# Performance work log

Measured on AMD Instinct MI355X. Metric: run time of the kernel, lower is better.

## Reference

```python
import jax, jax.numpy as jnp
import numpy as np

B, S, D = 2, 2048, 512
H = 8
HD = D // H  # head dim = 64


def setup_inputs() -> dict:
    key = jax.random.key(0)
    ks = jax.random.split(key, 4)
    scale = 1.0 / np.sqrt(D)
    x = jax.random.normal(ks[0], (B, S, D), dtype=jnp.float32)
    wq = jax.random.normal(ks[1], (D, D), dtype=jnp.float32) * scale
    wk = jax.random.normal(ks[2], (D, D), dtype=jnp.float32) * scale
    wv = jax.random.normal(ks[3], (D, D), dtype=jnp.float32) * scale
    bq = jnp.zeros((D,), dtype=jnp.float32)
    bk = jnp.zeros((D,), dtype=jnp.float32)
    bv = jnp.zeros((D,), dtype=jnp.float32)
    return {"x": x, "wq": wq, "bq": bq, "wk": wk, "bk": bk, "wv": wv, "bv": bv}


def reference(x, wq, bq, wk, bk, wv, bv):
    # Linear projections (torch Linear: y = x @ W^T + b; weights here stored as [out,in])
    q = x @ wq.T + bq  # [B,S,D]
    k = x @ wk.T + bk
    v = x @ wv.T + bv
    # split heads -> [B,H,S,HD]
    q = q.reshape(B, S, H, HD).transpose(0, 2, 1, 3)
    k = k.reshape(B, S, H, HD).transpose(0, 2, 1, 3)
    v = v.reshape(B, S, H, HD).transpose(0, 2, 1, 3)
    # QK^T scores, scaled by 1/sqrt(head_dim)
    scores = jnp.einsum("bhqd,bhkd->bhqk", q, k) / jnp.sqrt(jnp.float32(HD))
    # softmax-free: elementwise sigmoid instead of softmax normalization
    attn = jax.nn.sigmoid(scores)  # [B,H,S,S] — the memory-bound intermediate
    out = jnp.einsum("bhqk,bhkd->bhqd", attn, v)
    # merge heads -> [B,S,D]
    return out.transpose(0, 2, 1, 3).reshape(B, S, D)
```

## Files before the change

### kernel.cpp

```cpp
#include <hip/hip_runtime.h>
#include <cstdint>
#include <cstddef>

#define BB   2
#define SS   2048
#define DD   512
#define HH   8
#define HDIM 64
#define XN   ((size_t)BB * SS * DD)
#define WN   ((size_t)DD * DD)

typedef __attribute__((ext_vector_type(8)))  short          s16x8;
typedef __attribute__((ext_vector_type(8)))  unsigned short u16x8;
typedef __attribute__((ext_vector_type(16))) float          f32x16;

static __device__ __forceinline__ unsigned short f2bf(float f) {
  union { float f; unsigned u; } x; x.f = f;
  unsigned r = x.u + 0x7fffu + ((x.u >> 16) & 1u);
  return (unsigned short)(r >> 16);
}
static __device__ __forceinline__ unsigned packtrunc(float lo, float hi) {
  return __builtin_amdgcn_perm(__float_as_uint(hi), __float_as_uint(lo), 0x07060302u);
}

#define QSCALE (-0.18033688011111543f)

__global__ __launch_bounds__(256) void cvt_kernel(
    const float* __restrict__ x,
    const float* __restrict__ wq, const float* __restrict__ wk, const float* __restrict__ wv,
    unsigned short* __restrict__ xb, unsigned short* __restrict__ wb3) {
  const int y = blockIdx.y;
  const float* src; unsigned short* dst;
  if (y == 0) { src = x; dst = xb; }
  else {
    if (blockIdx.x >= 256) return;
    src = (y == 1) ? wq : (y == 2) ? wk : wv;
    dst = wb3 + (size_t)(y - 1) * WN;
  }
  int i = (blockIdx.x * 256 + threadIdx.x) * 4;
  float4 f = *(const float4*)(src + i);
  ushort4 o;
  o.x = f2bf(f.x); o.y = f2bf(f.y); o.z = f2bf(f.z); o.w = f2bf(f.w);
  *(ushort4*)(dst + i) = o;
}

__global__ __launch_bounds__(256) void proj_kernel(
    const unsigned short* __restrict__ xb, const unsigned short* __restrict__ wb3,
    const float* __restrict__ bq, const float* __restrict__ bk, const float* __restrict__ bv,
    unsigned short* __restrict__ qo, unsigned short* __restrict__ ko,
    unsigned short* __restrict__ vt) {
  __shared__ unsigned short As[2][128 * 40];
  __shared__ unsigned short Bs[2][64 * 40];

  const int z = blockIdx.z;
  const unsigned short* w = wb3 + (size_t)z * WN;
  const float* bias = (z == 0) ? bq : (z == 1) ? bk : bv;

  const int t = threadIdx.x;
  const int lane = t & 63, wave = t >> 6;
  const int ln = lane & 31, hi = lane >> 5;
  const int m0 = blockIdx.x * 128, n0 = blockIdx.y * 64;

  u16x8 ar[2], br;
#pragma unroll
  for (int i = 0; i < 2; i++) {
    int c = t + i * 256;
    ar[i] = *(const u16x8*)&xb[(size_t)(m0 + (c >> 2)) * DD + (c & 3) * 8];
  }
  br = *(const u16x8*)&w[(size_t)(n0 + (t >> 2)) * DD + (t & 3) * 8];
#pragma unroll
  for (int i = 0; i < 2; i++) {
    int c = t + i * 256;
    *(u16x8*)&As[0][(c >> 2) * 40 + (c & 3) * 8] = ar[i];
  }
  *(u16x8*)&Bs[0][(t >> 2) * 40 + (t & 3) * 8] = br;
  __syncthreads();

  f32x16 acc0 = {}, acc1 = {};

#pragma unroll 2
  for (int kt = 0; kt < 16; kt++) {
    const int cur = kt & 1, nxt = cur ^ 1;
    if (kt < 15) {
      int k0 = (kt + 1) * 32;
#pragma unroll
      for (int i = 0; i < 2; i++) {
        int c = t + i * 256;
        ar[i] = *(const u16x8*)&xb[(size_t)(m0 + (c >> 2)) * DD + k0 + (c & 3) * 8];
      }
      br = *(const u16x8*)&w[(size_t)(n0 + (t >> 2)) * DD + k0 + (t & 3) * 8];
    }
#pragma unroll
    for (int cc = 0; cc < 2; cc++) {
      s16x8 af = *(const s16x8*)&As[cur][(wave * 32 + ln) * 40 + cc * 16 + hi * 8];
      s16x8 b0 = *(const s16x8*)&Bs[cur][(ln) * 40 + cc * 16 + hi * 8];
      s16x8 b1 = *(const s16x8*)&Bs[cur][(32 + ln) * 40 + cc * 16 + hi * 8];
      acc0 = __builtin_amdgcn_mfma_f32_32x32x16_bf16(af, b0, acc0, 0, 0, 0);
      acc1 = __builtin_amdgcn_mfma_f32_32x32x16_bf16(af, b1, acc1, 0, 0, 0);
    }
    if (kt < 15) {
#pragma unroll
      for (int i = 0; i < 2; i++) {
        int c = t + i * 256;
        *(u16x8*)&As[nxt][(c >> 2) * 40 + (c & 3) * 8] = ar[i];
      }
      *(u16x8*)&Bs[nxt][(t >> 2) * 40 + (t & 3) * 8] = br;
    }
    __syncthreads();
  }

  const int h = blockIdx.y;
  const int bidx = m0 >> 11;
  const int sbase = (m0 & 2047) + wave * 32;
  const size_t bhb = (size_t)(bidx * HH + h) * SS * HDIM;
  const int kts = sbase >> 5;

#pragma unroll
  for (int nh = 0; nh < 2; nh++) {
    f32x16 acc = nh ? acc1 : acc0;
    const int hd = nh * 32 + ln;
    const float bval = bias[n0 + hd];

    if (z == 0) {
#pragma unroll
      for (int r = 0; r < 16; r++) {
        int s = sbase + (r & 3) + 8 * (r >> 2) + 4 * hi;
        qo[bhb + (size_t)s * HDIM + hd] = f2bf((acc[r] + bval) * QSCALE);
      }
    } else if (z == 1) {
      const int c = hd >> 4, hk = (hd >> 3) & 1, j = hd & 7;
      unsigned short* kd = ko + bhb + ((size_t)kts * 4 + c) * 512 + j;
#pragma unroll
      for (int r = 0; r < 16; r++) {
        int off = (r & 3) + 8 * (r >> 2) + 4 * hi;
        kd[(hk * 32 + off) * 8] = f2bf(acc[r] + bval);
      }
    } else {
      unsigned short* vd = vt + bhb + ((size_t)kts * 4 + nh * 2) * 512 + hi * 256 + ln * 8;
#pragma unroll
      for (int g = 0; g < 4; g++) {
        unsigned short* vg = vd + (g >> 1) * 512 + (g & 1) * 4;
#pragma unroll
        for (int j = 0; j < 4; j += 2) {
          unsigned pk = (unsigned)f2bf(acc[g * 4 + j] + bval) |
                        ((unsigned)f2bf(acc[g * 4 + j + 1] + bval) << 16);
          *(unsigned*)&vg[j] = pk;
        }
      }
    }
  }
}

__global__ __launch_bounds__(512, 2) void attn_kernel(
    const unsigned short* __restrict__ qb,
    const unsigned short* __restrict__ kfb,
    const unsigned short* __restrict__ vfb,
    float* __restrict__ out) {
  __shared__ __align__(16) float red[2 * 8192];

  const int t = threadIdx.x;
  const int lane = t & 63, wave = t >> 6;
  const int ln = lane & 31, hi = lane >> 5;
  const int qp = wave & 1, kh = wave >> 1;
  const int fid = blockIdx.y * 16 + blockIdx.x;
  const int bh = fid & 15, qx = fid >> 4;
  const int b = bh >> 3, h = bh & 7;
  const unsigned short* qp_ = qb + (size_t)bh * SS * HDIM;
  const unsigned short* kfp = kfb + (size_t)bh * SS * HDIM;
  const unsigned short* vfp = vfb + (size_t)bh * SS * HDIM;
  const int q0 = qx * 128 + qp * 64;

  s16x8 qf[2][4];
#pragma unroll
  for (int qs = 0; qs < 2; qs++)
#pragma unroll
    for (int c = 0; c < 4; c++)
      qf[qs][c] = *(const s16x8*)&qp_[(size_t)(q0 + qs * 32 + ln) * HDIM + c * 16 + hi * 8];

  f32x16 o00 = {}, o01 = {}, o10 = {}, o11 = {};

  s16x8 kf[4], vf[4];
  int foff = kh * 16 * 2048 + lane * 8;
#pragma unroll
  for (int c = 0; c < 4; c++) {
    kf[c] = *(const s16x8*)&kfp[foff + c * 512];
    vf[c] = *(const s16x8*)&vfp[foff + c * 512];
  }
  foff += 2048;

#pragma unroll 1
  for (int i = 0; i < 16; i++) {
    f32x16 st0 = {}, st1 = {};
#pragma unroll
    for (int c = 0; c < 4; c++) {
      st0 = __builtin_amdgcn_mfma_f32_32x32x16_bf16(kf[c], qf[0][c], st0, 0, 0, 0);
      st1 = __builtin_amdgcn_mfma_f32_32x32x16_bf16(kf[c], qf[1][c], st1, 0, 0, 0);
    }

    if (i < 15) {
#pragma unroll
      for (int c = 0; c < 4; c++)
        kf[c] = *(const s16x8*)&kfp[foff + c * 512];
    }

    unsigned pg[2][8];
#pragma unroll
    for (int qs = 0; qs < 2; qs++) {
      f32x16 st = qs ? st1 : st0;
#pragma unroll
      for (int g = 0; g < 4; g++) {
        float p0 = __builtin_amdgcn_rcpf(1.0f + __builtin_amdgcn_exp2f(st[4 * g + 0]));
        float p1 = __builtin_amdgcn_rcpf(1.0f + __builtin_amdgcn_exp2f(st[4 * g + 1]));
        float p2 = __builtin_amdgcn_rcpf(1.0f + __builtin_amdgcn_exp2f(st[4 * g + 2]));
        float p3 = __builtin_amdgcn_rcpf(1.0f + __builtin_amdgcn_exp2f(st[4 * g + 3]));
        pg[qs][2 * g]     = packtrunc(p0, p1);
        pg[qs][2 * g + 1] = packtrunc(p2, p3);
      }
    }

#pragma unroll
    for (int c = 0; c < 2; c++) {
#pragma unroll
      for (int qs = 0; qs < 2; qs++) {
        union { unsigned u[4]; s16x8 v; } pu;
        pu.u[0] = pg[qs][4 * c + 0];
        pu.u[1] = pg[qs][4 * c + 1];
        pu.u[2] = pg[qs][4 * c + 2];
        pu.u[3] = pg[qs][4 * c + 3];
        if (qs == 0) {
          o00 = __builtin_amdgcn_mfma_f32_32x32x16_bf16(pu.v, vf[c], o00, 0, 0, 0);
          o01 = __builtin_amdgcn_mfma_f32_32x32x16_bf16(pu.v, vf[2 + c], o01, 0, 0, 0);
        } else {
          o10 = __builtin_amdgcn_mfma_f32_32x32x16_bf16(pu.v, vf[c], o10, 0, 0, 0);
          o11 = __builtin_amdgcn_mfma_f32_32x32x16_bf16(pu.v, vf[2 + c], o11, 0, 0, 0);
        }
      }
    }

    if (i < 15) {
#pragma unroll
      for (int c = 0; c < 4; c++)
        vf[c] = *(const s16x8*)&vfp[foff + c * 512];
      foff += 2048;
    }
  }

  if (kh >= 2) {
    float* slot = red + (kh - 2) * 8192;
#pragma unroll
    for (int qs = 0; qs < 2; qs++)
#pragma unroll
      for (int dh = 0; dh < 2; dh++) {
        f32x16 ov = qs ? (dh ? o11 : o10) : (dh ? o01 : o00);
#pragma unroll
        for (int r = 0; r < 16; r++) {
          int ql = qp * 64 + qs * 32 + (r & 3) + 8 * (r >> 2) + 4 * hi;
          slot[ql * 64 + dh * 32 + ln] = ov[r];
        }
      }
  }
  __syncthreads();
  if (kh < 2) {
    float* slot = red + kh * 8192;
#pragma unroll
    for (int qs = 0; qs < 2; qs++)
#pragma unroll
      for (int dh = 0; dh < 2; dh++) {
        f32x16 ov = qs ? (dh ? o11 : o10) : (dh ? o01 : o00);
#pragma unroll
        for (int r = 0; r < 16; r++) {
          int ql = qp * 64 + qs * 32 + (r & 3) + 8 * (r >> 2) + 4 * hi;
          slot[ql * 64 + dh * 32 + ln] += ov[r];
        }
      }
  }
  __syncthreads();
  const float4* r0 = (const float4*)red;
  const float4* r1 = (const float4*)(red + 8192);
  const int qblk = qx * 128;
#pragma unroll
  for (int j = 0; j < 4; j++) {
    int g = t + j * 512;
    float4 s0 = r0[g], s1 = r1[g];
    float4 s;
    s.x = s0.x + s1.x; s.y = s0.y + s1.y; s.z = s0.z + s1.z; s.w = s0.w + s1.w;
    int q = g >> 4, dbase = (g & 15) * 4;
    *(float4*)&out[((size_t)(b * SS + qblk + q)) * DD + h * HDIM + dbase] = s;
  }
}

extern "C" void kernel_launch(void* const* d_in, const int* in_sizes, int n_in,
                              void* d_out, int out_size, void* d_ws, size_t ws_size,
                              hipStream_t stream) {
  const float* x  = (const float*)d_in[0];
  const float* wq = (const float*)d_in[1];
  const float* bq = (const float*)d_in[2];
  const float* wk = (const float*)d_in[3];
  const float* bk = (const float*)d_in[4];
  const float* wv = (const float*)d_in[5];
  const float* bv = (const float*)d_in[6];
  float* out = (float*)d_out;

  unsigned short* xb = (unsigned short*)d_ws;
  unsigned short* wb = xb + XN;
  unsigned short* qo = wb + 3 * WN;
  unsigned short* ko = qo + XN;
  unsigned short* vt = ko + XN;

  cvt_kernel<<<dim3(2048, 4), 256, 0, stream>>>(x, wq, wk, wv, xb, wb);
  proj_kernel<<<dim3(32, 8, 3), 256, 0, stream>>>(xb, wb, bq, bk, bv, qo, ko, vt);
  attn_kernel<<<dim3(SS / 128, BB * HH), 512, 0, stream>>>(qo, ko, vt, out);
}
```

Baseline: 113.1 us.

## Fuse x fp32-to-bf16 conversion into projection and compute Q/K/V per block

The projection kernel now reads fp32 x directly and converts it to bf16 while staging tiles into shared memory, so the separate x conversion pass and its bf16 workspace round trip go away. Each block also computes all three Q, K and V projections from one shared A tile instead of launching a z dimension of 3, which reuses the loaded x tile three times. In exchange the grid shrinks from 768 to 256 blocks, each holding six accumulators and triple B buffers, which raises register and LDS pressure (launch bounds now ask for one block per CU) and may reduce occupancy.

```diff
diff --git a/kernel.cpp b/kernel.cpp
--- a/kernel.cpp
+++ b/kernel.cpp
@@ -25,18 +25,12 @@
 
 #define QSCALE (-0.18033688011111543f)
 
-__global__ __launch_bounds__(256) void cvt_kernel(
-    const float* __restrict__ x,
+__global__ __launch_bounds__(256) void cvtw_kernel(
     const float* __restrict__ wq, const float* __restrict__ wk, const float* __restrict__ wv,
-    unsigned short* __restrict__ xb, unsigned short* __restrict__ wb3) {
-  const int y = blockIdx.y;
-  const float* src; unsigned short* dst;
-  if (y == 0) { src = x; dst = xb; }
-  else {
-    if (blockIdx.x >= 256) return;
-    src = (y == 1) ? wq : (y == 2) ? wk : wv;
-    dst = wb3 + (size_t)(y - 1) * WN;
-  }
+    unsigned short* __restrict__ wb3) {
+  const int z = blockIdx.y;
+  const float* src = (z == 0) ? wq : (z == 1) ? wk : wv;
+  unsigned short* dst = wb3 + (size_t)z * WN;
   int i = (blockIdx.x * 256 + threadIdx.x) * 4;
   float4 f = *(const float4*)(src + i);
   ushort4 o;
@@ -44,39 +38,51 @@
   *(ushort4*)(dst + i) = o;
 }
 
-__global__ __launch_bounds__(256) void proj_kernel(
-    const unsigned short* __restrict__ xb, const unsigned short* __restrict__ wb3,
+__global__ __launch_bounds__(256, 1) void proj_kernel(
+    const float* __restrict__ x, const unsigned short* __restrict__ wb3,
     const float* __restrict__ bq, const float* __restrict__ bk, const float* __restrict__ bv,
     unsigned short* __restrict__ qo, unsigned short* __restrict__ ko,
     unsigned short* __restrict__ vt) {
   __shared__ unsigned short As[2][128 * 40];
-  __shared__ unsigned short Bs[2][64 * 40];
-
-  const int z = blockIdx.z;
-  const unsigned short* w = wb3 + (size_t)z * WN;
-  const float* bias = (z == 0) ? bq : (z == 1) ? bk : bv;
+  __shared__ unsigned short Bs[2][3][64 * 40];
 
   const int t = threadIdx.x;
   const int lane = t & 63, wave = t >> 6;
   const int ln = lane & 31, hi = lane >> 5;
   const int m0 = blockIdx.x * 128, n0 = blockIdx.y * 64;
 
-  u16x8 ar[2], br;
+  float4 axf[2][2];
+  u16x8 br[3];
 #pragma unroll
   for (int i = 0; i < 2; i++) {
     int c = t + i * 256;
-    ar[i] = *(const u16x8*)&xb[(size_t)(m0 + (c >> 2)) * DD + (c & 3) * 8];
-  }
-  br = *(const u16x8*)&w[(size_t)(n0 + (t >> 2)) * DD + (t & 3) * 8];
+    const float* ap = x + (size_t)(m0 + (c >> 2)) * DD + (c & 3) * 8;
+    axf[i][0] = *(const float4*)ap;
+    axf[i][1] = *(const float4*)(ap + 4);
+  }
+#pragma unroll
+  for (int z = 0; z < 3; z++)
+    br[z] = *(const u16x8*)&wb3[(size_t)z * WN + (size_t)(n0 + (t >> 2)) * DD + (t & 3) * 8];
+
 #pragma unroll
   for (int i = 0; i < 2; i++) {
     int c = t + i * 256;
-    *(u16x8*)&As[0][(c >> 2) * 40 + (c & 3) * 8] = ar[i];
-  }
-  *(u16x8*)&Bs[0][(t >> 2) * 40 + (t & 3) * 8] = br;
+    u16x8 ar;
+#pragma unroll
+    for (int j = 0; j < 4; j++) {
+      ar[j]     = f2bf(((const float*)&axf[i][0])[j]);
+      ar[4 + j] = f2bf(((const float*)&axf[i][1])[j]);
+    }
+    *(u16x8*)&As[0][(c >> 2) * 40 + (c & 3) * 8] = ar;
+  }
+#pragma unroll
+  for (int z = 0; z < 3; z++)
+    *(u16x8*)&Bs[0][z][(t >> 2) * 40 + (t & 3) * 8] = br[z];
   __syncthreads();
 
-  f32x16 acc0 = {}, acc1 = {};
+  f32x16 acc[3][2];
+#pragma unroll
+  for (int z = 0; z < 3; z++) { acc[z][0] = (f32x16){}; acc[z][1] = (f32x16){}; }
 
 #pragma unroll 2
   for (int kt = 0; kt < 16; kt++) {
@@ -86,25 +92,40 @@
 #pragma unroll
       for (int i = 0; i < 2; i++) {
         int c = t + i * 256;
-        ar[i] = *(const u16x8*)&xb[(size_t)(m0 + (c >> 2)) * DD + k0 + (c & 3) * 8];
-      }
-      br = *(const u16x8*)&w[(size_t)(n0 + (t >> 2)) * DD + k0 + (t & 3) * 8];
+        const float* ap = x + (size_t)(m0 + (c >> 2)) * DD + k0 + (c & 3) * 8;
+        axf[i][0] = *(const float4*)ap;
+        axf[i][1] = *(const float4*)(ap + 4);
+      }
+#pragma unroll
+      for (int z = 0; z < 3; z++)
+        br[z] = *(const u16x8*)&wb3[(size_t)z * WN + (size_t)(n0 + (t >> 2)) * DD + k0 + (t & 3) * 8];
     }
 #pragma unroll
     for (int cc = 0; cc < 2; cc++) {
       s16x8 af = *(const s16x8*)&As[cur][(wave * 32 + ln) * 40 + cc * 16 + hi * 8];
-      s16x8 b0 = *(const s16x8*)&Bs[cur][(ln) * 40 + cc * 16 + hi * 8];
-      s16x8 b1 = *(const s16x8*)&Bs[cur][(32 + ln) * 40 + cc * 16 + hi * 8];
-      acc0 = __builtin_amdgcn_mfma_f32_32x32x16_bf16(af, b0, acc0, 0, 0, 0);
-      acc1 = __builtin_amdgcn_mfma_f32_32x32x16_bf16(af, b1, acc1, 0, 0, 0);
+#pragma unroll
+      for (int z = 0; z < 3; z++) {
+        s16x8 b0 = *(const s16x8*)&Bs[cur][z][(ln) * 40 + cc * 16 + hi * 8];
+        s16x8 b1 = *(const s16x8*)&Bs[cur][z][(32 + ln) * 40 + cc * 16 + hi * 8];
+        acc[z][0] = __builtin_amdgcn_mfma_f32_32x32x16_bf16(af, b0, acc[z][0], 0, 0, 0);
+        acc[z][1] = __builtin_amdgcn_mfma_f32_32x32x16_bf16(af, b1, acc[z][1], 0, 0, 0);
+      }
     }
     if (kt < 15) {
 #pragma unroll
       for (int i = 0; i < 2; i++) {
         int c = t + i * 256;
-        *(u16x8*)&As[nxt][(c >> 2) * 40 + (c & 3) * 8] = ar[i];
-      }
-      *(u16x8*)&Bs[nxt][(t >> 2) * 40 + (t & 3) * 8] = br;
+        u16x8 ar;
+#pragma unroll
+        for (int j = 0; j < 4; j++) {
+          ar[j]     = f2bf(((const float*)&axf[i][0])[j]);
+          ar[4 + j] = f2bf(((const float*)&axf[i][1])[j]);
+        }
+        *(u16x8*)&As[nxt][(c >> 2) * 40 + (c & 3) * 8] = ar;
+      }
+#pragma unroll
+      for (int z = 0; z < 3; z++)
+        *(u16x8*)&Bs[nxt][z][(t >> 2) * 40 + (t & 3) * 8] = br[z];
     }
     __syncthreads();
   }
@@ -117,34 +138,39 @@
 
 #pragma unroll
   for (int nh = 0; nh < 2; nh++) {
-    f32x16 acc = nh ? acc1 : acc0;
     const int hd = nh * 32 + ln;
-    const float bval = bias[n0 + hd];
-
-    if (z == 0) {
+    {
+      f32x16 av = acc[0][nh];
+      const float bval = bq[n0 + hd];
 #pragma unroll
       for (int r = 0; r < 16; r++) {
         int s = sbase + (r & 3) + 8 * (r >> 2) + 4 * hi;
-        qo[bhb + (size_t)s * HDIM + hd] = f2bf((acc[r] + bval) * QSCALE);
-      }
-    } else if (z == 1) {
+        qo[bhb + (size_t)s * HDIM + hd] = f2bf((av[r] + bval) * QSCALE);
+      }
+    }
+    {
+      f32x16 av = acc[1][nh];
+      const float bval = bk[n0 + hd];
       const int c = hd >> 4, hk = (hd >> 3) & 1, j = hd & 7;
       unsigned short* kd = ko + bhb + ((size_t)kts * 4 + c) * 512 + j;
 #pragma unroll
       for (int r = 0; r < 16; r++) {
         int off = (r & 3) + 8 * (r >> 2) + 4 * hi;
-        kd[(hk * 32 + off) * 8] = f2bf(acc[r] + bval);
-      }
-    } else {
+        kd[(hk * 32 + off) * 8] = f2bf(av[r] + bval);
+      }
+    }
+    {
+      f32x16 av = acc[2][nh];
+      const float bval = bv[n0 + hd];
       unsigned short* vd = vt + bhb + ((size_t)kts * 4 + nh * 2) * 512 + hi * 256 + ln * 8;
 #pragma unroll
       for (int g = 0; g < 4; g++) {
         unsigned short* vg = vd + (g >> 1) * 512 + (g & 1) * 4;
 #pragma unroll
-        for (int j = 0; j < 4; j += 2) {
-          unsigned pk = (unsigned)f2bf(acc[g * 4 + j] + bval) |
-                        ((unsigned)f2bf(acc[g * 4 + j + 1] + bval) << 16);
-          *(unsigned*)&vg[j] = pk;
+        for (int j2 = 0; j2 < 4; j2 += 2) {
+          unsigned pk = (unsigned)f2bf(av[g * 4 + j2] + bval) |
+                        ((unsigned)f2bf(av[g * 4 + j2 + 1] + bval) << 16);
+          *(unsigned*)&vg[j2] = pk;
         }
       }
     }
@@ -301,13 +327,12 @@
   const float* bv = (const float*)d_in[6];
   float* out = (float*)d_out;
 
-  unsigned short* xb = (unsigned short*)d_ws;
-  unsigned short* wb = xb + XN;
+  unsigned short* wb = (unsigned short*)d_ws;
   unsigned short* qo = wb + 3 * WN;
   unsigned short* ko = qo + XN;
   unsigned short* vt = ko + XN;
 
-  cvt_kernel<<<dim3(2048, 4), 256, 0, stream>>>(x, wq, wk, wv, xb, wb);
-  proj_kernel<<<dim3(32, 8, 3), 256, 0, stream>>>(xb, wb, bq, bk, bv, qo, ko, vt);
+  cvtw_kernel<<<dim3(256, 3), 256, 0, stream>>>(wq, wk, wv, wb);
+  proj_kernel<<<dim3(32, 8), 256, 0, stream>>>(x, wb, bq, bk, bv, qo, ko, vt);
   attn_kernel<<<dim3(SS / 128, BB * HH), 512, 0, stream>>>(qo, ko, vt, out);
 }
```

Result: no change. 113.4 us (+0.3%).
